# Performance work log

Hardware: AMD Instinct MI355X
Metric: run time of the kernel (lower is better)

Reference implementation:

```python
import jax, jax.numpy as jnp
import numpy as np
import math

R1 = 1.0
R2 = 4.0
NBINS_XY = 4
NBINS_ZY = 4
PARTITIONS = NBINS_XY * NBINS_ZY * 2  # 32
TOPK = 200
TWO_PI = 2.0 * math.pi
PI = math.pi


def setup_inputs() -> dict:
    key = jax.random.key(0)
    k1, k2 = jax.random.split(key)
    # LiDAR-like coordinates, ~[-30, 30] meters
    sampled_vehicle_points = jax.random.normal(k1, (1024, 3), dtype=jnp.float32) * 20.0
    fusion_point = jax.random.normal(k2, (20000, 3), dtype=jnp.float32) * 20.0
    return {"sampled_vehicle_points": sampled_vehicle_points, "fusion_point": fusion_point}


def _compute_partitions_batch(q):
    # q: [S, K, 3]. rel[b, i, j] = q[b, j] - q[b, i]  (A.unsqueeze(1) - B.unsqueeze(2))
    rel = q[:, None, :, :] - q[:, :, None, :]  # [S, K, K, 3]
    angles_xy = jnp.fmod(jnp.arctan2(rel[..., 1], rel[..., 0]) + TWO_PI, TWO_PI)
    angles_zy = jnp.fmod(jnp.arctan2(rel[..., 1], rel[..., 2]) + TWO_PI, PI)
    xy_bins = jnp.floor(angles_xy / (TWO_PI / NBINS_XY))
    zy_bins = jnp.floor(angles_zy / (PI / NBINS_ZY))
    # hash(A, B, seed=NBINS_ZY): -1 where either < 0
    angle_ok = (xy_bins >= 0) & (zy_bins >= 0)
    angles_bins = jnp.where(angle_ok, xy_bins * NBINS_ZY + zy_bins, -1.0)
    D = jnp.sqrt(jnp.sum(rel * rel, axis=-1) + 1e-7)  # [S, K, K]
    dist_bins = jnp.where(D >= R2, 1.0, jnp.where(D >= R1, 0.0, -1.0))
    bin_ok = (dist_bins >= 0) & (angles_bins >= 0)
    bins = jnp.where(bin_ok, dist_bins * (NBINS_XY * NBINS_ZY) + angles_bins, -1.0)
    return bins  # [S, K, K] float, -1 for ignored


def reference(sampled_vehicle_points, fusion_point):
    # kNN query: K nearest fusion points for each sampled vehicle point
    d2 = jnp.sum(
        (sampled_vehicle_points[:, None, :] - fusion_point[None, :, :]) ** 2, axis=-1
    )  # [S, Nf]
    _, idx = jax.lax.top_k(-d2, TOPK)  # indices of TOPK smallest distances
    queried = fusion_point[idx]  # [S, K, 3]

    bins = _compute_partitions_batch(queried)  # [S, K, K]
    row0 = bins[:, 0, :]  # [S, K] — only row 0 is used by the loss
    # points_in_partition[s, p] = sum_j (row0[s, j] == p) + 1
    counts = jnp.sum(
        row0[:, :, None] == jnp.arange(PARTITIONS, dtype=bins.dtype)[None, None, :],
        axis=1,
    ).astype(jnp.float32) + 1.0  # [S, P]
    pip = counts / jnp.linalg.norm(counts, axis=-1, keepdims=True) * 4.0
    gt_dist = jax.nn.softmax(pip, axis=-1)
    return gt_dist
```

## Files before the change

kernel.cpp:

```cpp
#include <hip/hip_runtime.h>
#include <math.h>

#define KTOP 200
#define NPART 32
#define BLOCK 512
#define NHIST 2048
#define CAND_CAP 512
#define WCAP 512
#define MAXIT 10

__device__ __forceinline__ float d2_ref(float ax, float ay, float az,
                                        float bx, float by, float bz) {
    float dx = __fsub_rn(ax, bx), dy = __fsub_rn(ay, by), dz = __fsub_rn(az, bz);
    return __fadd_rn(__fadd_rn(__fmul_rn(dx, dx), __fmul_rn(dy, dy)), __fmul_rn(dz, dz));
}

__device__ __forceinline__ unsigned key_of(const float* __restrict__ fus, int j,
                                           float vx, float vy, float vz) {
    return __float_as_uint(d2_ref(vx, vy, vz, fus[3*j], fus[3*j+1], fus[3*j+2]));
}

__device__ __forceinline__ int compute_bin(float rx, float ry, float rz) {
    const float TWO_PI_F = (float)6.283185307179586;
    const float PI_F     = (float)3.141592653589793;
    const float XY_W     = (float)(6.283185307179586 / 4.0);
    const float ZY_W     = (float)(3.141592653589793 / 4.0);

    float d2 = __fadd_rn(__fadd_rn(__fmul_rn(rx, rx), __fmul_rn(ry, ry)), __fmul_rn(rz, rz));
    float D  = sqrtf(__fadd_rn(d2, 1e-7f));
    float dist_bin;
    if (D >= 4.0f)      dist_bin = 1.0f;
    else if (D >= 1.0f) dist_bin = 0.0f;
    else                return -1;

    float axy = fmodf(atan2f(ry, rx) + TWO_PI_F, TWO_PI_F);
    float azy = fmodf(atan2f(ry, rz) + TWO_PI_F, PI_F);
    float xyb = floorf(__fdiv_rn(axy, XY_W));
    float zyb = floorf(__fdiv_rn(azy, ZY_W));
    if (!(xyb >= 0.0f && zyb >= 0.0f)) return -1;
    float ab  = xyb * 4.0f + zyb;
    int bin = (int)(dist_bin * 16.0f + ab);
    return bin;
}

__global__ __launch_bounds__(BLOCK, 8)
void shape_context_kernel(const float* __restrict__ veh,
                          const float* __restrict__ fus,
                          float* __restrict__ out,
                          int nfus) {
    const int b   = blockIdx.x;
    const int tid = threadIdx.x;
    const int lane = tid & 63;
    const int wid  = tid >> 6;

    __shared__ unsigned int hist[NHIST];
    __shared__ unsigned long long cand[CAND_CAP];
    __shared__ int wlist[WCAP];
    __shared__ unsigned int hist32[NPART];
    __shared__ unsigned int waveTot[BLOCK / 64];
    __shared__ unsigned int waveBase[BLOCK / 64];
    __shared__ unsigned int s_bucket, s_rem, s_bcount;
    __shared__ int s_candCount, s_wcount;
    __shared__ float s_q0[3];
    __shared__ unsigned long long s_minPacked, s_lowBound;

    const float vx = veh[b * 3 + 0], vy = veh[b * 3 + 1], vz = veh[b * 3 + 2];
    const float4* fus4 = (const float4*)fus;
    const int ntrip = nfus >> 2;

    if (tid == 0) { s_minPacked = ~0ull; s_candCount = 0; s_wcount = 0; }
    for (int i = tid; i < NHIST; i += BLOCK) hist[i] = 0;
    if (tid < NPART) hist32[tid] = 0;
    __syncthreads();

    auto find_bucket = [&](unsigned remq) {
        const int PER = NHIST / BLOCK;
        int base = tid * PER;
        unsigned p = 0;
        #pragma unroll
        for (int i = 0; i < PER; i++) p += hist[base + i];
        unsigned incl = p;
        #pragma unroll
        for (int d = 1; d < 64; d <<= 1) {
            unsigned n = __shfl_up(incl, d, 64);
            if (lane >= d) incl += n;
        }
        if (lane == 63) waveTot[wid] = incl;
        __syncthreads();
        if (tid == 0) {
            unsigned acc = 0;
            for (int w = 0; w < BLOCK / 64; w++) { waveBase[w] = acc; acc += waveTot[w]; }
        }
        __syncthreads();
        unsigned excl = waveBase[wid] + incl - p;
        if (excl < remq && remq <= excl + p) {
            unsigned cum = excl;
            #pragma unroll
            for (int i = 0; i < PER; i++) {
                unsigned c = hist[base + i];
                if (cum + c >= remq) { s_bucket = base + i; s_rem = remq - cum; s_bcount = c; break; }
                cum += c;
            }
        }
        __syncthreads();
    };

    unsigned long long khi[MAXIT];
    unsigned long long lmin = ~0ull;
    #pragma unroll
    for (int it = 0; it < MAXIT; ++it) {
        int m = tid + it * BLOCK;
        if (m < ntrip) {
            float4 A = fus4[3 * m], Bq = fus4[3 * m + 1], Cq = fus4[3 * m + 2];
            unsigned k0 = __float_as_uint(d2_ref(vx, vy, vz, A.x,  A.y,  A.z));
            unsigned k1 = __float_as_uint(d2_ref(vx, vy, vz, A.w,  Bq.x, Bq.y));
            unsigned k2 = __float_as_uint(d2_ref(vx, vy, vz, Bq.z, Bq.w, Cq.x));
            unsigned k3 = __float_as_uint(d2_ref(vx, vy, vz, Cq.y, Cq.z, Cq.w));
            atomicAdd(&hist[k0 >> 21], 1u);
            atomicAdd(&hist[k1 >> 21], 1u);
            atomicAdd(&hist[k2 >> 21], 1u);
            atomicAdd(&hist[k3 >> 21], 1u);
            khi[it] = (unsigned long long)(k0 >> 21)
                    | ((unsigned long long)(k1 >> 21) << 16)
                    | ((unsigned long long)(k2 >> 21) << 32)
                    | ((unsigned long long)(k3 >> 21) << 48);
            unsigned jb = 4 * m;
            unsigned long long p0 = ((unsigned long long)k0 << 32) | (jb + 0);
            unsigned long long p1 = ((unsigned long long)k1 << 32) | (jb + 1);
            unsigned long long p2 = ((unsigned long long)k2 << 32) | (jb + 2);
            unsigned long long p3 = ((unsigned long long)k3 << 32) | (jb + 3);
            unsigned long long pm = min(min(p0, p1), min(p2, p3));
            lmin = min(lmin, pm);
        } else {
            khi[it] = 0xFFFFFFFFFFFFFFFFull;
        }
    }
    for (int m = MAXIT * BLOCK + tid; m < ntrip; m += BLOCK) {
        #pragma unroll
        for (int q = 0; q < 4; ++q) {
            unsigned k = key_of(fus, 4 * m + q, vx, vy, vz);
            atomicAdd(&hist[k >> 21], 1u);
            lmin = min(lmin, ((unsigned long long)k << 32) | (unsigned)(4 * m + q));
        }
    }
    for (int j = (nfus & ~3) + tid; j < nfus; j += BLOCK) {
        unsigned k = key_of(fus, j, vx, vy, vz);
        atomicAdd(&hist[k >> 21], 1u);
        lmin = min(lmin, ((unsigned long long)k << 32) | (unsigned)j);
    }
    #pragma unroll
    for (int d = 32; d > 0; d >>= 1) {
        unsigned long long o = __shfl_xor(lmin, d, 64);
        lmin = (o < lmin) ? o : lmin;
    }
    if (lane == 0) atomicMin(&s_minPacked, lmin);
    __syncthreads();

    find_bucket(KTOP);
    unsigned T = s_bucket;
    unsigned rem = s_rem;
    unsigned bcount = s_bcount;
    int shift = 21;

    if (tid == 0) {
        int idx0 = (int)(s_minPacked & 0xFFFFFFFFull);
        s_q0[0] = fus[idx0 * 3]; s_q0[1] = fus[idx0 * 3 + 1]; s_q0[2] = fus[idx0 * 3 + 2];
    }
    __syncthreads();
    const float q0x = s_q0[0], q0y = s_q0[1], q0z = s_q0[2];

    while (bcount > CAND_CAP && shift > 0) {
        int newshift = (shift > 11) ? (shift - 11) : 0;
        unsigned digmask = (1u << (shift - newshift)) - 1;
        for (int i = tid; i < NHIST; i += BLOCK) hist[i] = 0;
        __syncthreads();
        for (int j = tid; j < nfus; j += BLOCK) {
            unsigned k = key_of(fus, j, vx, vy, vz);
            if ((k >> shift) == T) atomicAdd(&hist[(k >> newshift) & digmask], 1u);
        }
        __syncthreads();
        find_bucket(rem);
        T = (T << (shift - newshift)) | s_bucket;
        rem = s_rem;
        bcount = s_bcount;
        shift = newshift;
    }

    if (shift == 21) {
        #pragma unroll
        for (int it = 0; it < MAXIT; ++it) {
            unsigned long long packed = khi[it];
            int jb = 4 * (tid + it * BLOCK);
            #pragma unroll
            for (int q = 0; q < 4; ++q) {
                unsigned hi = (unsigned)((packed >> (16 * q)) & 0xFFFFull);
                if (hi < T) {
                    int pos = atomicAdd(&s_wcount, 1);
                    if (pos < WCAP) wlist[pos] = jb + q;
                } else if (hi == T) {
                    int j = jb + q;
                    unsigned k = key_of(fus, j, vx, vy, vz);
                    int pos = atomicAdd(&s_candCount, 1);
                    if (pos < CAND_CAP) cand[pos] = ((unsigned long long)k << 32) | (unsigned)j;
                }
            }
        }
        for (int m = MAXIT * BLOCK + tid; m < ntrip; m += BLOCK)
            #pragma unroll
            for (int q = 0; q < 4; ++q) {
                int j = 4 * m + q;
                unsigned k = key_of(fus, j, vx, vy, vz);
                unsigned hi = k >> shift;
                if (hi < T) { int pos = atomicAdd(&s_wcount, 1); if (pos < WCAP) wlist[pos] = j; }
                else if (hi == T) { int pos = atomicAdd(&s_candCount, 1); if (pos < CAND_CAP) cand[pos] = ((unsigned long long)k << 32) | (unsigned)j; }
            }
        for (int j = (nfus & ~3) + tid; j < nfus; j += BLOCK) {
            unsigned k = key_of(fus, j, vx, vy, vz);
            unsigned hi = k >> shift;
            if (hi < T) { int pos = atomicAdd(&s_wcount, 1); if (pos < WCAP) wlist[pos] = j; }
            else if (hi == T) { int pos = atomicAdd(&s_candCount, 1); if (pos < CAND_CAP) cand[pos] = ((unsigned long long)k << 32) | (unsigned)j; }
        }
    } else {
        for (int j = tid; j < nfus; j += BLOCK) {
            unsigned k = key_of(fus, j, vx, vy, vz);
            unsigned hi = k >> shift;
            if (hi < T) { int pos = atomicAdd(&s_wcount, 1); if (pos < WCAP) wlist[pos] = j; }
            else if (hi == T) { int pos = atomicAdd(&s_candCount, 1); if (pos < CAND_CAP) cand[pos] = ((unsigned long long)k << 32) | (unsigned)j; }
        }
    }
    __syncthreads();

    const int cnt = s_candCount;
    if (cnt <= CAND_CAP) {
        for (int i = tid; i < cnt; i += BLOCK) {
            unsigned long long me = cand[i];
            int rank = 0;
            for (int k2 = 0; k2 < cnt; k2++) rank += (cand[k2] < me) ? 1 : 0;
            if (rank < (int)rem) {
                int pos = atomicAdd(&s_wcount, 1);
                if (pos < WCAP) wlist[pos] = (int)(me & 0xFFFFFFFFull);
            }
        }
    }
    __syncthreads();

    {
        int wc = s_wcount; if (wc > WCAP) wc = WCAP;
        for (int i = tid; i < wc; i += BLOCK) {
            int j = wlist[i];
            float fx = fus[3 * j], fy = fus[3 * j + 1], fz = fus[3 * j + 2];
            int bin = compute_bin(__fsub_rn(fx, q0x), __fsub_rn(fy, q0y), __fsub_rn(fz, q0z));
            if (bin >= 0 && bin < NPART) atomicAdd(&hist32[bin], 1u);
        }
    }
    __syncthreads();

    if (cnt > CAND_CAP) {
        if (tid == 0) s_lowBound = 0;
        __syncthreads();
        for (unsigned itx = 0; itx < rem; ++itx) {
            if (tid == 0) s_minPacked = ~0ull;
            __syncthreads();
            unsigned long long lowB = s_lowBound;
            unsigned long long lm = ~0ull;
            for (int j = tid; j < nfus; j += BLOCK) {
                unsigned k = key_of(fus, j, vx, vy, vz);
                if ((k >> shift) == T) {
                    unsigned long long p = ((unsigned long long)k << 32) | (unsigned)j;
                    if (p >= lowB && p < lm) lm = p;
                }
            }
            #pragma unroll
            for (int d = 32; d > 0; d >>= 1) {
                unsigned long long o = __shfl_xor(lm, d, 64);
                lm = (o < lm) ? o : lm;
            }
            if (lane == 0) atomicMin(&s_minPacked, lm);
            __syncthreads();
            if (tid == 0) {
                int jm = (int)(s_minPacked & 0xFFFFFFFFull);
                float fx = fus[jm * 3], fy = fus[jm * 3 + 1], fz = fus[jm * 3 + 2];
                int bin = compute_bin(__fsub_rn(fx, q0x), __fsub_rn(fy, q0y), __fsub_rn(fz, q0z));
                if (bin >= 0 && bin < NPART) hist32[bin] += 1u;
                s_lowBound = s_minPacked + 1;
            }
            __syncthreads();
        }
    }

    if (tid < NPART) {
        float c = (float)hist32[tid] + 1.0f;
        float ss = __fmul_rn(c, c);
        #pragma unroll
        for (int d = 16; d > 0; d >>= 1) ss += __shfl_xor(ss, d, 64);
        float v = __fmul_rn(__fdiv_rn(c, sqrtf(ss)), 4.0f);
        float mx = v;
        #pragma unroll
        for (int d = 16; d > 0; d >>= 1) mx = fmaxf(mx, __shfl_xor(mx, d, 64));
        float e = expf(v - mx);
        float sum = e;
        #pragma unroll
        for (int d = 16; d > 0; d >>= 1) sum += __shfl_xor(sum, d, 64);
        out[b * NPART + tid] = __fdiv_rn(e, sum);
    }
}

extern "C" void kernel_launch(void* const* d_in, const int* in_sizes, int n_in,
                              void* d_out, int out_size, void* d_ws, size_t ws_size,
                              hipStream_t stream) {
    const float* veh = (const float*)d_in[0];
    const float* fus = (const float*)d_in[1];
    float* out = (float*)d_out;
    int nveh = in_sizes[0] / 3;
    int nfus = in_sizes[1] / 3;
    shape_context_kernel<<<nveh, BLOCK, 0, stream>>>(veh, fus, out, nfus);
}
```

Measured before the change: 82.77 us.

## Sample first chunk to bound histogram and compact candidate list in shared memory

Uses the first 2048 points to estimate a histogram bucket threshold E that should contain the top-K. Remaining points are only histogrammed and appended to a shared-memory candidate list if they fall at or below E, so the final selection pass scans this short list instead of all points. Per-thread register arrays of packed keys are removed. A fallback rebuilds the full histogram when the list overflows or the bucket exceeds E, which adds complexity and an extra shared buffer that may reduce occupancy.

```diff
diff --git a/kernel.cpp b/kernel.cpp
--- a/kernel.cpp
+++ b/kernel.cpp
@@ -7,7 +7,8 @@
 #define NHIST 2048
 #define CAND_CAP 512
 #define WCAP 512
-#define MAXIT 10
+#define CLIST_CAP 1536
+#define SRANK_MIN 64u
 
 __device__ __forceinline__ float d2_ref(float ax, float ay, float az,
                                         float bx, float by, float bz) {
@@ -54,13 +55,14 @@
     const int wid  = tid >> 6;
 
     __shared__ unsigned int hist[NHIST];
+    __shared__ unsigned long long clist[CLIST_CAP];
     __shared__ unsigned long long cand[CAND_CAP];
     __shared__ int wlist[WCAP];
     __shared__ unsigned int hist32[NPART];
     __shared__ unsigned int waveTot[BLOCK / 64];
     __shared__ unsigned int waveBase[BLOCK / 64];
     __shared__ unsigned int s_bucket, s_rem, s_bcount;
-    __shared__ int s_candCount, s_wcount;
+    __shared__ int s_candCount, s_wcount, s_clistCount;
     __shared__ float s_q0[3];
     __shared__ unsigned long long s_minPacked, s_lowBound;
 
@@ -68,12 +70,13 @@
     const float4* fus4 = (const float4*)fus;
     const int ntrip = nfus >> 2;
 
-    if (tid == 0) { s_minPacked = ~0ull; s_candCount = 0; s_wcount = 0; }
+    if (tid == 0) { s_minPacked = ~0ull; s_candCount = 0; s_wcount = 0; s_clistCount = 0; }
     for (int i = tid; i < NHIST; i += BLOCK) hist[i] = 0;
     if (tid < NPART) hist32[tid] = 0;
     __syncthreads();
 
     auto find_bucket = [&](unsigned remq) {
+        if (tid == 0) s_bucket = 0xFFFFFFFFu;
         const int PER = NHIST / BLOCK;
         int base = tid * PER;
         unsigned p = 0;
@@ -105,49 +108,72 @@
         __syncthreads();
     };
 
-    unsigned long long khi[MAXIT];
     unsigned long long lmin = ~0ull;
-    #pragma unroll
-    for (int it = 0; it < MAXIT; ++it) {
-        int m = tid + it * BLOCK;
-        if (m < ntrip) {
-            float4 A = fus4[3 * m], Bq = fus4[3 * m + 1], Cq = fus4[3 * m + 2];
-            unsigned k0 = __float_as_uint(d2_ref(vx, vy, vz, A.x,  A.y,  A.z));
-            unsigned k1 = __float_as_uint(d2_ref(vx, vy, vz, A.w,  Bq.x, Bq.y));
-            unsigned k2 = __float_as_uint(d2_ref(vx, vy, vz, Bq.z, Bq.w, Cq.x));
-            unsigned k3 = __float_as_uint(d2_ref(vx, vy, vz, Cq.y, Cq.z, Cq.w));
-            atomicAdd(&hist[k0 >> 21], 1u);
-            atomicAdd(&hist[k1 >> 21], 1u);
-            atomicAdd(&hist[k2 >> 21], 1u);
-            atomicAdd(&hist[k3 >> 21], 1u);
-            khi[it] = (unsigned long long)(k0 >> 21)
-                    | ((unsigned long long)(k1 >> 21) << 16)
-                    | ((unsigned long long)(k2 >> 21) << 32)
-                    | ((unsigned long long)(k3 >> 21) << 48);
-            unsigned jb = 4 * m;
-            unsigned long long p0 = ((unsigned long long)k0 << 32) | (jb + 0);
-            unsigned long long p1 = ((unsigned long long)k1 << 32) | (jb + 1);
-            unsigned long long p2 = ((unsigned long long)k2 << 32) | (jb + 2);
-            unsigned long long p3 = ((unsigned long long)k3 << 32) | (jb + 3);
-            unsigned long long pm = min(min(p0, p1), min(p2, p3));
-            lmin = min(lmin, pm);
+    unsigned k0 = 0, k1 = 0, k2 = 0, k3 = 0;
+    const bool t0v = (tid < ntrip);
+    if (t0v) {
+        float4 A = fus4[3 * tid], Bq = fus4[3 * tid + 1], Cq = fus4[3 * tid + 2];
+        k0 = __float_as_uint(d2_ref(vx, vy, vz, A.x,  A.y,  A.z));
+        k1 = __float_as_uint(d2_ref(vx, vy, vz, A.w,  Bq.x, Bq.y));
+        k2 = __float_as_uint(d2_ref(vx, vy, vz, Bq.z, Bq.w, Cq.x));
+        k3 = __float_as_uint(d2_ref(vx, vy, vz, Cq.y, Cq.z, Cq.w));
+        atomicAdd(&hist[k0 >> 21], 1u);
+        atomicAdd(&hist[k1 >> 21], 1u);
+        atomicAdd(&hist[k2 >> 21], 1u);
+        atomicAdd(&hist[k3 >> 21], 1u);
+        unsigned jb = 4u * (unsigned)tid;
+        unsigned long long p0 = ((unsigned long long)k0 << 32) | (jb + 0);
+        unsigned long long p1 = ((unsigned long long)k1 << 32) | (jb + 1);
+        unsigned long long p2 = ((unsigned long long)k2 << 32) | (jb + 2);
+        unsigned long long p3 = ((unsigned long long)k3 << 32) | (jb + 3);
+        lmin = min(min(p0, p1), min(p2, p3));
+    }
+    __syncthreads();
+
+    unsigned srank;
+    {
+        long long sample = (long long)((ntrip < BLOCK) ? ntrip : BLOCK) * 4;
+        if (sample >= (long long)nfus) {
+            srank = KTOP;
         } else {
-            khi[it] = 0xFFFFFFFFFFFFFFFFull;
-        }
-    }
-    for (int m = MAXIT * BLOCK + tid; m < ntrip; m += BLOCK) {
-        #pragma unroll
-        for (int q = 0; q < 4; ++q) {
-            unsigned k = key_of(fus, 4 * m + q, vx, vy, vz);
-            atomicAdd(&hist[k >> 21], 1u);
-            lmin = min(lmin, ((unsigned long long)k << 32) | (unsigned)(4 * m + q));
-        }
+            unsigned s2 = (unsigned)(((long long)3 * KTOP * sample + nfus - 1) / nfus);
+            srank = (s2 < SRANK_MIN) ? SRANK_MIN : s2;
+        }
+    }
+    find_bucket(srank);
+    const unsigned E = (s_bucket < NHIST) ? s_bucket : (NHIST - 1);
+
+    if (t0v) {
+        unsigned jb = 4u * (unsigned)tid;
+        if ((k0 >> 21) <= E) { int pos = atomicAdd(&s_clistCount, 1); if (pos < CLIST_CAP) clist[pos] = ((unsigned long long)k0 << 32) | (jb + 0); }
+        if ((k1 >> 21) <= E) { int pos = atomicAdd(&s_clistCount, 1); if (pos < CLIST_CAP) clist[pos] = ((unsigned long long)k1 << 32) | (jb + 1); }
+        if ((k2 >> 21) <= E) { int pos = atomicAdd(&s_clistCount, 1); if (pos < CLIST_CAP) clist[pos] = ((unsigned long long)k2 << 32) | (jb + 2); }
+        if ((k3 >> 21) <= E) { int pos = atomicAdd(&s_clistCount, 1); if (pos < CLIST_CAP) clist[pos] = ((unsigned long long)k3 << 32) | (jb + 3); }
+    }
+
+    for (int m = BLOCK + tid; m < ntrip; m += BLOCK) {
+        float4 A = fus4[3 * m], Bq = fus4[3 * m + 1], Cq = fus4[3 * m + 2];
+        unsigned q0k = __float_as_uint(d2_ref(vx, vy, vz, A.x,  A.y,  A.z));
+        unsigned q1k = __float_as_uint(d2_ref(vx, vy, vz, A.w,  Bq.x, Bq.y));
+        unsigned q2k = __float_as_uint(d2_ref(vx, vy, vz, Bq.z, Bq.w, Cq.x));
+        unsigned q3k = __float_as_uint(d2_ref(vx, vy, vz, Cq.y, Cq.z, Cq.w));
+        unsigned jb = 4u * (unsigned)m;
+        unsigned long long p0 = ((unsigned long long)q0k << 32) | (jb + 0);
+        unsigned long long p1 = ((unsigned long long)q1k << 32) | (jb + 1);
+        unsigned long long p2 = ((unsigned long long)q2k << 32) | (jb + 2);
+        unsigned long long p3 = ((unsigned long long)q3k << 32) | (jb + 3);
+        lmin = min(lmin, min(min(p0, p1), min(p2, p3)));
+        if ((q0k >> 21) <= E) { atomicAdd(&hist[q0k >> 21], 1u); int pos = atomicAdd(&s_clistCount, 1); if (pos < CLIST_CAP) clist[pos] = p0; }
+        if ((q1k >> 21) <= E) { atomicAdd(&hist[q1k >> 21], 1u); int pos = atomicAdd(&s_clistCount, 1); if (pos < CLIST_CAP) clist[pos] = p1; }
+        if ((q2k >> 21) <= E) { atomicAdd(&hist[q2k >> 21], 1u); int pos = atomicAdd(&s_clistCount, 1); if (pos < CLIST_CAP) clist[pos] = p2; }
+        if ((q3k >> 21) <= E) { atomicAdd(&hist[q3k >> 21], 1u); int pos = atomicAdd(&s_clistCount, 1); if (pos < CLIST_CAP) clist[pos] = p3; }
     }
     for (int j = (nfus & ~3) + tid; j < nfus; j += BLOCK) {
         unsigned k = key_of(fus, j, vx, vy, vz);
-        atomicAdd(&hist[k >> 21], 1u);
         lmin = min(lmin, ((unsigned long long)k << 32) | (unsigned)j);
-    }
+        if ((k >> 21) <= E) { atomicAdd(&hist[k >> 21], 1u); int pos = atomicAdd(&s_clistCount, 1); if (pos < CLIST_CAP) clist[pos] = ((unsigned long long)k << 32) | (unsigned)j; }
+    }
+
     #pragma unroll
     for (int d = 32; d > 0; d >>= 1) {
         unsigned long long o = __shfl_xor(lmin, d, 64);
@@ -161,6 +187,7 @@
     unsigned rem = s_rem;
     unsigned bcount = s_bcount;
     int shift = 21;
+    const bool fastOK = (s_clistCount <= CLIST_CAP) && (T <= E);
 
     if (tid == 0) {
         int idx0 = (int)(s_minPacked & 0xFFFFFFFFull);
@@ -168,6 +195,18 @@
     }
     __syncthreads();
     const float q0x = s_q0[0], q0y = s_q0[1], q0z = s_q0[2];
+
+    if (!fastOK) {
+        for (int i = tid; i < NHIST; i += BLOCK) hist[i] = 0;
+        __syncthreads();
+        for (int j = tid; j < nfus; j += BLOCK) {
+            unsigned k = key_of(fus, j, vx, vy, vz);
+            atomicAdd(&hist[k >> 21], 1u);
+        }
+        __syncthreads();
+        find_bucket(KTOP);
+        T = s_bucket; rem = s_rem; bcount = s_bcount;
+    }
 
     while (bcount > CAND_CAP && shift > 0) {
         int newshift = (shift > 11) ? (shift - 11) : 0;
@@ -186,39 +225,18 @@
         shift = newshift;
     }
 
-    if (shift == 21) {
-        #pragma unroll
-        for (int it = 0; it < MAXIT; ++it) {
-            unsigned long long packed = khi[it];
-            int jb = 4 * (tid + it * BLOCK);
-            #pragma unroll
-            for (int q = 0; q < 4; ++q) {
-                unsigned hi = (unsigned)((packed >> (16 * q)) & 0xFFFFull);
-                if (hi < T) {
-                    int pos = atomicAdd(&s_wcount, 1);
-                    if (pos < WCAP) wlist[pos] = jb + q;
-                } else if (hi == T) {
-                    int j = jb + q;
-                    unsigned k = key_of(fus, j, vx, vy, vz);
-                    int pos = atomicAdd(&s_candCount, 1);
-                    if (pos < CAND_CAP) cand[pos] = ((unsigned long long)k << 32) | (unsigned)j;
-                }
-            }
-        }
-        for (int m = MAXIT * BLOCK + tid; m < ntrip; m += BLOCK)
-            #pragma unroll
-            for (int q = 0; q < 4; ++q) {
-                int j = 4 * m + q;
-                unsigned k = key_of(fus, j, vx, vy, vz);
-                unsigned hi = k >> shift;
-                if (hi < T) { int pos = atomicAdd(&s_wcount, 1); if (pos < WCAP) wlist[pos] = j; }
-                else if (hi == T) { int pos = atomicAdd(&s_candCount, 1); if (pos < CAND_CAP) cand[pos] = ((unsigned long long)k << 32) | (unsigned)j; }
-            }
-        for (int j = (nfus & ~3) + tid; j < nfus; j += BLOCK) {
-            unsigned k = key_of(fus, j, vx, vy, vz);
-            unsigned hi = k >> shift;
-            if (hi < T) { int pos = atomicAdd(&s_wcount, 1); if (pos < WCAP) wlist[pos] = j; }
-            else if (hi == T) { int pos = atomicAdd(&s_candCount, 1); if (pos < CAND_CAP) cand[pos] = ((unsigned long long)k << 32) | (unsigned)j; }
+    if (fastOK && shift == 21) {
+        const int cn = s_clistCount;
+        for (int i = tid; i < cn; i += BLOCK) {
+            unsigned long long p = clist[i];
+            unsigned hi = (unsigned)(p >> 53);
+            if (hi < T) {
+                int pos = atomicAdd(&s_wcount, 1);
+                if (pos < WCAP) wlist[pos] = (int)(p & 0xFFFFFFFFull);
+            } else if (hi == T) {
+                int pos = atomicAdd(&s_candCount, 1);
+                if (pos < CAND_CAP) cand[pos] = p;
+            }
         }
     } else {
         for (int j = tid; j < nfus; j += BLOCK) {
```

Result: faster. 75.78 us (-8.5%).
